# Performance work log

Hardware: AMD Instinct MI355X
Metric: run time of the kernel (lower is better)

The kernel has to match this reference:

```python
import jax, jax.numpy as jnp
import numpy as np

B, NQ, NK = 2, 4096, 4096
DQ = DK = DV = 256
H = 8
DH = DV // H  # 32
LN_EPS = 1e-5


def _layer_norm(x, gamma, beta):
    mu = jnp.mean(x, axis=-1, keepdims=True)
    var = jnp.var(x, axis=-1, keepdims=True)
    return (x - mu) * jax.lax.rsqrt(var + LN_EPS) * gamma + beta


def setup_inputs() -> dict:
    key = jax.random.key(0)
    ks = jax.random.split(key, 12)
    s = 0.02
    return {
        "Q": jax.random.normal(ks[0], (B, NQ, DQ), jnp.float32),
        "K": jax.random.normal(ks[1], (B, NK, DK), jnp.float32),
        "Wq": jax.random.normal(ks[2], (DV, DQ), jnp.float32) * s,
        "bq": jnp.zeros((DV,), jnp.float32),
        "Wk": jax.random.normal(ks[3], (DV, DK), jnp.float32) * s,
        "bk": jnp.zeros((DV,), jnp.float32),
        "Wv": jax.random.normal(ks[4], (DV, DK), jnp.float32) * s,
        "bv": jnp.zeros((DV,), jnp.float32),
        "Wo": jax.random.normal(ks[5], (DV, DV), jnp.float32) * s,
        "bo": jnp.zeros((DV,), jnp.float32),
        "g0": jnp.ones((DV,), jnp.float32),
        "beta0": jnp.zeros((DV,), jnp.float32),
        "g1": jnp.ones((DV,), jnp.float32),
        "beta1": jnp.zeros((DV,), jnp.float32),
    }


def reference(Q, K, Wq, bq, Wk, bk, Wv, bv, Wo, bo, g0, beta0, g1, beta1):
    # dropout is identity in eval mode
    b, nq, _ = Q.shape
    nk = K.shape[1]
    Qp = (Q @ Wq.T + bq).reshape(b, nq, H, DH)
    Kp = (K @ Wk.T + bk).reshape(b, nk, H, DH)
    Vp = (K @ Wv.T + bv).reshape(b, nk, H, DH)
    scale = 1.0 / np.sqrt(DH).astype(np.float32)
    scores = jnp.einsum("bqhd,bkhd->bhqk", Qp, Kp) * scale
    attn = jax.nn.softmax(scores, axis=-1)
    out = jnp.einsum("bhqk,bkhd->bqhd", attn, Vp).reshape(b, nq, DV)
    out = out @ Wo.T + bo
    out = _layer_norm(out, g0, beta0)
    out = _layer_norm(out + jax.nn.relu(out), g1, beta1)
    return out
```

## Files before the change

### kernel.cpp

```cpp
#include <hip/hip_runtime.h>
#include <hip/hip_bf16.h>
#include <math.h>


typedef __attribute__((ext_vector_type(4))) float f32x4;
typedef __attribute__((ext_vector_type(16))) float f32x16;
typedef __attribute__((ext_vector_type(8))) short s16x8;
typedef __attribute__((ext_vector_type(2))) unsigned u32x2;

#define MFMA_BF16(A, B, C) __builtin_amdgcn_mfma_f32_16x16x32_bf16((A), (B), (C), 0, 0, 0)
#define MFMA32(A, B, C) __builtin_amdgcn_mfma_f32_32x32x16_bf16((A), (B), (C), 0, 0, 0)

static __device__ __forceinline__ unsigned short f2bf(float f) {
    union { float f; unsigned u; } v; v.f = f;
    unsigned u = v.u;
    unsigned r = (u + 0x7FFFu + ((u >> 16) & 1u)) >> 16;
    return (unsigned short)r;
}

static __device__ __forceinline__ float bf2f(unsigned short b) {
    union { unsigned u; float f; } v; v.u = ((unsigned)b) << 16;
    return v.f;
}

static __device__ __forceinline__ unsigned cvtpk(float lo, float hi) {
    unsigned r;
    asm("v_cvt_pk_bf16_f32 %0, %1, %2" : "=v"(r) : "v"(lo), "v"(hi));
    return r;
}

static __device__ __forceinline__ s16x8 mk8(unsigned a, unsigned b, unsigned c, unsigned d) {
    union { unsigned u[4]; s16x8 v; } x;
    x.u[0] = a; x.u[1] = b; x.u[2] = c; x.u[3] = d;
    return x.v;
}

__global__ __launch_bounds__(256) void k_cvt_all(
    const float* __restrict__ K,
    const float* __restrict__ Wq, const float* __restrict__ Wk,
    const float* __restrict__ Wv, const float* __restrict__ Wo,
    unsigned short* __restrict__ Kb,
    unsigned short* __restrict__ Wqf, unsigned short* __restrict__ Wkf,
    unsigned short* __restrict__ Wvf, unsigned short* __restrict__ Wof) {
    int bid = blockIdx.x, tid = threadIdx.x;
    if (bid < 2048) {
        int idx = bid * 256 + tid;
        float4 v = ((const float4*)K)[idx];
        ushort4 o;
        o.x = f2bf(v.x); o.y = f2bf(v.y); o.z = f2bf(v.z); o.w = f2bf(v.w);
        ((ushort4*)Kb)[idx] = o;
    } else {
        int w = (bid - 2048) >> 6;
        const float* src = (w == 0) ? Wq : (w == 1) ? Wk : (w == 2) ? Wv : Wo;
        unsigned short* dst = (w == 0) ? Wqf : (w == 1) ? Wkf : (w == 2) ? Wvf : Wof;
        int idx = ((bid - 2048) & 63) * 256 + tid;
        int s = idx * 4;
        int row = s >> 8, col = s & 255;
        float4 v = ((const float4*)src)[idx];
        size_t d = (size_t)(row >> 4) * 4096 + ((size_t)(col >> 5) << 9) +
                   (((col >> 3) & 3) << 7) + ((row & 15) << 3) + (col & 7);
        ushort4 o;
        o.x = f2bf(v.x); o.y = f2bf(v.y); o.z = f2bf(v.z); o.w = f2bf(v.w);
        *(ushort4*)(dst + d) = o;
    }
}

__global__ __launch_bounds__(128) void k_proj(
    const float* __restrict__ Qf, const unsigned short* __restrict__ Kb,
    const unsigned short* __restrict__ Wqf, const unsigned short* __restrict__ Wkf,
    const unsigned short* __restrict__ Wvf,
    const float* __restrict__ bq, const float* __restrict__ bk, const float* __restrict__ bv,
    unsigned short* __restrict__ Qp, unsigned short* __restrict__ Kf,
    unsigned short* __restrict__ Vf, float qscale) {
    __shared__ unsigned short lds[2][16][256];
    const int wv = threadIdx.x >> 6, lid = threadIdx.x & 63;
    const int i = lid & 15, G = lid >> 4;
    const int bid = blockIdx.x;
    if (bid < 512) {
        const int which = bid >> 8;
        const unsigned short* W = which ? Wkf : Wqf;
        const float* bias = which ? bk : bq;
        const float scale = which ? 1.0f : qscale;
        const int m0 = (bid & 255) * 32 + wv * 16;
        f32x4 acc[16];
#pragma unroll
        for (int nf = 0; nf < 16; ++nf) acc[nf] = f32x4{0.f, 0.f, 0.f, 0.f};
        const unsigned short* Xrow = Kb + (size_t)(m0 + i) * 256;
        const float* Qrow = Qf + (size_t)(m0 + i) * 256;
#pragma unroll
        for (int k0 = 0; k0 < 256; k0 += 32) {
            s16x8 a;
            if (which) {
                a = *(const s16x8*)(Xrow + k0 + G * 8);
            } else {
                float4 f0 = *(const float4*)(Qrow + k0 + G * 8);
                float4 f1 = *(const float4*)(Qrow + k0 + G * 8 + 4);
                a = mk8(cvtpk(f0.x, f0.y), cvtpk(f0.z, f0.w),
                        cvtpk(f1.x, f1.y), cvtpk(f1.z, f1.w));
            }
#pragma unroll
            for (int nf = 0; nf < 16; ++nf) {
                s16x8 b = *(const s16x8*)(W + nf * 4096 + ((k0 >> 5) << 9) + lid * 8);
                acc[nf] = MFMA_BF16(a, b, acc[nf]);
            }
        }
#pragma unroll
        for (int nf = 0; nf < 16; ++nf) {
            int col = nf * 16 + i;
            float bvv = bias[col];
#pragma unroll
            for (int r = 0; r < 4; ++r) {
                lds[wv][G * 4 + r][col] = f2bf((acc[nf][r] + bvv) * scale);
            }
        }
#pragma unroll
        for (int it = 0; it < 8; ++it) {
            int run = it * 64 + lid;
            int row = run >> 5, cg = run & 31;
            int col0 = cg * 8;
            s16x8 v = *(const s16x8*)&lds[wv][row][col0];
            int m = m0 + row;
            int bb = m >> 12, j = m & 4095;
            int h = col0 >> 5, dh0 = col0 & 31;
            if (which == 0) {
                *(s16x8*)(Qp + (size_t)(((bb << 3) + h) * 4096 + j) * 32 + dh0) = v;
            } else {
                size_t off = (size_t)((bb << 3) + h) * 131072 +
                             (size_t)(j >> 5) * 1024 + ((dh0 >> 4) & 1) * 512 +
                             ((j & 31) + ((dh0 >> 3) & 1) * 32) * 8;
                *(s16x8*)(Kf + off) = v;
            }
        }
    } else {
        const int tid = bid - 512;
        const int n0 = (tid & 127) * 64;
        const int dv0 = (tid >> 7) * 32 + wv * 16;
        f32x4 acc[4];
#pragma unroll
        for (int nf = 0; nf < 4; ++nf) acc[nf] = f32x4{0.f, 0.f, 0.f, 0.f};
        const unsigned short* Wvp = Wvf + (size_t)((tid >> 7) * 2 + wv) * 4096;
#pragma unroll
        for (int k0 = 0; k0 < 256; k0 += 32) {
            s16x8 a = *(const s16x8*)(Wvp + ((k0 >> 5) << 9) + lid * 8);
#pragma unroll
            for (int nf = 0; nf < 4; ++nf) {
                s16x8 b = *(const s16x8*)(Kb + (size_t)(n0 + nf * 16 + i) * 256 + k0 + G * 8);
                acc[nf] = MFMA_BF16(a, b, acc[nf]);
            }
        }
#pragma unroll
        for (int r = 0; r < 4; ++r) {
            float bvv = bv[dv0 + G * 4 + r];
#pragma unroll
            for (int nf = 0; nf < 4; ++nf) {
                lds[wv][G * 4 + r][nf * 16 + i] = f2bf(acc[nf][r] + bvv);
            }
        }
#pragma unroll
        for (int it = 0; it < 2; ++it) {
            int run = it * 64 + lid;
            int row = run >> 3, jg = run & 7;
            int j0l = jg * 8;
            s16x8 v = *(const s16x8*)&lds[wv][row][j0l];
            int dv = dv0 + row;
            int j = n0 + j0l;
            int bb = j >> 12, jj = j & 4095;
            int h = dv >> 5, dvl = dv & 31;
            int rem = jj & 31;
            size_t off = (size_t)((bb << 3) + h) * 131072 +
                         (size_t)(jj >> 5) * 1024 + (rem >> 4) * 512 +
                         (size_t)(dvl + ((rem >> 3) & 1) * 32) * 8;
            *(s16x8*)(Vf + off) = v;
        }
    }
}

static __device__ __forceinline__ void sm_tile(f32x16 st, s16x8& pa0, s16x8& pa1) {
#pragma unroll
    for (int r = 0; r < 16; ++r) st[r] = __builtin_amdgcn_exp2f(st[r]);
    unsigned w00 = cvtpk(st[0], st[1]),   w01 = cvtpk(st[2], st[3]);
    unsigned w10 = cvtpk(st[4], st[5]),   w11 = cvtpk(st[6], st[7]);
    unsigned w20 = cvtpk(st[8], st[9]),   w21 = cvtpk(st[10], st[11]);
    unsigned w30 = cvtpk(st[12], st[13]), w31 = cvtpk(st[14], st[15]);
    u32x2 sA0 = __builtin_amdgcn_permlane32_swap(w00, w10, false, false);
    u32x2 sB0 = __builtin_amdgcn_permlane32_swap(w01, w11, false, false);
    u32x2 sA1 = __builtin_amdgcn_permlane32_swap(w20, w30, false, false);
    u32x2 sB1 = __builtin_amdgcn_permlane32_swap(w21, w31, false, false);
    pa0 = mk8(sA0[0], sB0[0], sA0[1], sB0[1]);
    pa1 = mk8(sA1[0], sB1[0], sA1[1], sB1[1]);
}

__global__ __launch_bounds__(256, 4) void k_attn(const unsigned short* __restrict__ Qp,
                                                 const unsigned short* __restrict__ Kf,
                                                 const unsigned short* __restrict__ Vf,
                                                 unsigned short* __restrict__ Ob,
                                                 float* __restrict__ Lb) {
    const int wv = threadIdx.x >> 6, l = threadIdx.x & 63;
    const int ql = l & 31, hi = l >> 5;
    int bid = blockIdx.x;
    int wg = ((bid & 7) << 7) | (bid >> 3);
    int bh = wg >> 6;
    int rest = wg & 63;
    int qblk = rest >> 1, sp = rest & 1;
    const unsigned short* Qh = Qp + (size_t)bh * 4096 * 32;
    const int q0 = qblk * 128 + wv * 32;

    s16x8 qb0 = *(const s16x8*)(Qh + (size_t)(q0 + ql) * 32 + hi * 8);
    s16x8 qb1 = *(const s16x8*)(Qh + (size_t)(q0 + ql) * 32 + 16 + hi * 8);

    f32x16 acc, accL, Z;
#pragma unroll
    for (int r = 0; r < 16; ++r) { acc[r] = 0.f; accL[r] = 0.f; Z[r] = 0.f; }
    const s16x8 ONES = mk8(0x3F803F80u, 0x3F803F80u, 0x3F803F80u, 0x3F803F80u);

    const unsigned short* Kl = Kf + (size_t)bh * 131072 + (size_t)sp * 65536 + l * 8;
    const unsigned short* Vl = Vf + (size_t)bh * 131072 + (size_t)sp * 65536 + l * 8;
    s16x8 kA0 = *(const s16x8*)(Kl + 0),    kA1 = *(const s16x8*)(Kl + 512);
    s16x8 kB0 = *(const s16x8*)(Kl + 1024), kB1 = *(const s16x8*)(Kl + 1536);
    s16x8 vA0 = *(const s16x8*)(Vl + 0),    vA1 = *(const s16x8*)(Vl + 512);
    s16x8 vB0 = *(const s16x8*)(Vl + 1024), vB1 = *(const s16x8*)(Vl + 1536);

    f32x16 st = MFMA32(kA0, qb0, Z);
    st = MFMA32(kA1, qb1, st);
    s16x8 paA0, paA1, paB0, paB1;
    sm_tile(st, paA0, paA1);
    f32x16 stn;

    for (int t = 0; t < 64; t += 2) {
        {
            int t2 = (t + 2 < 64) ? t + 2 : 62;
            stn  = MFMA32(kB0, qb0, Z);
            stn  = MFMA32(kB1, qb1, stn);
            acc  = MFMA32(paA0, vA0, acc);
            acc  = MFMA32(paA1, vA1, acc);
            accL = MFMA32(paA0, ONES, accL);
            accL = MFMA32(paA1, ONES, accL);
            kA0 = *(const s16x8*)(Kl + (size_t)t2 * 1024);
            kA1 = *(const s16x8*)(Kl + (size_t)t2 * 1024 + 512);
            sm_tile(stn, paB0, paB1);
            vA0 = *(const s16x8*)(Vl + (size_t)t2 * 1024);
            vA1 = *(const s16x8*)(Vl + (size_t)t2 * 1024 + 512);
        }
        {
            int t2 = (t + 3 < 64) ? t + 3 : 62;
            stn  = MFMA32(kA0, qb0, Z);
            stn  = MFMA32(kA1, qb1, stn);
            acc  = MFMA32(paB0, vB0, acc);
            acc  = MFMA32(paB1, vB1, acc);
            accL = MFMA32(paB0, ONES, accL);
            accL = MFMA32(paB1, ONES, accL);
            kB0 = *(const s16x8*)(Kl + (size_t)t2 * 1024);
            kB1 = *(const s16x8*)(Kl + (size_t)t2 * 1024 + 512);
            sm_tile(stn, paA0, paA1);
            vB0 = *(const s16x8*)(Vl + (size_t)t2 * 1024);
            vB1 = *(const s16x8*)(Vl + (size_t)t2 * 1024 + 512);
        }
    }

    const int bb = bh >> 3, h = bh & 7;
    unsigned short* Obs = Ob + (size_t)sp * 8192 * 256;
#pragma unroll
    for (int r = 0; r < 16; ++r) {
        int qr = (r & 3) + 8 * (r >> 2) + 4 * hi;
        float o = acc[r] / accL[r];
        Obs[(size_t)((bb << 12) + q0 + qr) * 256 + h * 32 + ql] = f2bf(o);
        if (ql == 0) Lb[(size_t)(sp * 16 + bh) * 4096 + q0 + qr] = accL[r];
    }
}

__global__ __launch_bounds__(128) void k_epi(const unsigned short* __restrict__ Ob,
                                             const float* __restrict__ Lb,
                                             const unsigned short* __restrict__ W,
                                             const float* __restrict__ bo,
                                             const float* __restrict__ g0,
                                             const float* __restrict__ be0,
                                             const float* __restrict__ g1,
                                             const float* __restrict__ be1,
                                             float* __restrict__ out) {
    const int wv = threadIdx.x >> 6, lid = threadIdx.x & 63;
    const int i = lid & 15, G = lid >> 4;
    const int m0 = blockIdx.x * 32 + wv * 16;
    const int mrow = m0 + i;
    const int bb = mrow >> 12, qq = mrow & 4095;
    float lw0[8], lw1[8];
#pragma unroll
    for (int h = 0; h < 8; ++h) {
        float l0 = Lb[(size_t)(bb * 8 + h) * 4096 + qq];
        float l1 = Lb[(size_t)(16 + bb * 8 + h) * 4096 + qq];
        float inv = 1.f / (l0 + l1);
        lw0[h] = l0 * inv;
        lw1[h] = l1 * inv;
    }
    f32x4 acc[16];
#pragma unroll
    for (int nf = 0; nf < 16; ++nf) acc[nf] = f32x4{0.f, 0.f, 0.f, 0.f};
    const unsigned short* A0 = Ob + (size_t)mrow * 256;
    const unsigned short* A1 = Ob + (size_t)8192 * 256 + (size_t)mrow * 256;
#pragma unroll
    for (int k0 = 0; k0 < 256; k0 += 32) {
        int h = k0 >> 5;
        float w0 = lw0[h], w1 = lw1[h];
        s16x8 x0 = *(const s16x8*)(A0 + k0 + G * 8);
        s16x8 x1 = *(const s16x8*)(A1 + k0 + G * 8);
        union { unsigned short us[8]; s16x8 v; } au;
#pragma unroll
        for (int e = 0; e < 8; ++e) {
            float c = bf2f((unsigned short)x0[e]) * w0 + bf2f((unsigned short)x1[e]) * w1;
            au.us[e] = f2bf(c);
        }
        s16x8 a = au.v;
#pragma unroll
        for (int nf = 0; nf < 16; ++nf) {
            s16x8 b = *(const s16x8*)(W + nf * 4096 + ((k0 >> 5) << 9) + lid * 8);
            acc[nf] = MFMA_BF16(a, b, acc[nf]);
        }
    }
    f32x4 s1 = f32x4{0.f, 0.f, 0.f, 0.f}, s2 = f32x4{0.f, 0.f, 0.f, 0.f};
#pragma unroll
    for (int nf = 0; nf < 16; ++nf) {
        float bbv = bo[nf * 16 + i];
#pragma unroll
        for (int r = 0; r < 4; ++r) {
            float x = acc[nf][r] + bbv;
            acc[nf][r] = x;
            s1[r] += x;
            s2[r] += x * x;
        }
    }
#pragma unroll
    for (int mk = 1; mk < 16; mk <<= 1) {
#pragma unroll
        for (int r = 0; r < 4; ++r) {
            s1[r] += __shfl_xor(s1[r], mk);
            s2[r] += __shfl_xor(s2[r], mk);
        }
    }
    f32x4 mu, rs;
#pragma unroll
    for (int r = 0; r < 4; ++r) {
        mu[r] = s1[r] * (1.f / 256.f);
        float var = s2[r] * (1.f / 256.f) - mu[r] * mu[r];
        rs[r] = rsqrtf(var + 1e-5f);
    }
    f32x4 t1 = f32x4{0.f, 0.f, 0.f, 0.f}, t2 = f32x4{0.f, 0.f, 0.f, 0.f};
#pragma unroll
    for (int nf = 0; nf < 16; ++nf) {
        float gv = g0[nf * 16 + i], bv = be0[nf * 16 + i];
#pragma unroll
        for (int r = 0; r < 4; ++r) {
            float y = (acc[nf][r] - mu[r]) * rs[r] * gv + bv;
            float z = y + fmaxf(y, 0.f);
            acc[nf][r] = z;
            t1[r] += z;
            t2[r] += z * z;
        }
    }
#pragma unroll
    for (int mk = 1; mk < 16; mk <<= 1) {
#pragma unroll
        for (int r = 0; r < 4; ++r) {
            t1[r] += __shfl_xor(t1[r], mk);
            t2[r] += __shfl_xor(t2[r], mk);
        }
    }
    f32x4 mu2, rs2;
#pragma unroll
    for (int r = 0; r < 4; ++r) {
        mu2[r] = t1[r] * (1.f / 256.f);
        float var = t2[r] * (1.f / 256.f) - mu2[r] * mu2[r];
        rs2[r] = rsqrtf(var + 1e-5f);
    }
#pragma unroll
    for (int nf = 0; nf < 16; ++nf) {
        int col = nf * 16 + i;
        float gv = g1[col], bv = be1[col];
#pragma unroll
        for (int r = 0; r < 4; ++r) {
            out[(size_t)(m0 + G * 4 + r) * 256 + col] = (acc[nf][r] - mu2[r]) * rs2[r] * gv + bv;
        }
    }
}

extern "C" void kernel_launch(void* const* d_in, const int* in_sizes, int n_in,
                              void* d_out, int out_size, void* d_ws, size_t ws_size,
                              hipStream_t stream) {
    const float* Q   = (const float*)d_in[0];
    const float* K   = (const float*)d_in[1];
    const float* Wq  = (const float*)d_in[2];
    const float* bq  = (const float*)d_in[3];
    const float* Wk  = (const float*)d_in[4];
    const float* bk  = (const float*)d_in[5];
    const float* Wv  = (const float*)d_in[6];
    const float* bv  = (const float*)d_in[7];
    const float* Wo  = (const float*)d_in[8];
    const float* bo  = (const float*)d_in[9];
    const float* g0  = (const float*)d_in[10];
    const float* be0 = (const float*)d_in[11];
    const float* g1  = (const float*)d_in[12];
    const float* be1 = (const float*)d_in[13];
    float* out = (float*)d_out;

    char* ws = (char*)d_ws;
    unsigned short* Wqf = (unsigned short*)(ws + (size_t)0);
    unsigned short* Wkf = (unsigned short*)(ws + ((size_t)128 << 10));
    unsigned short* Wvf = (unsigned short*)(ws + ((size_t)256 << 10));
    unsigned short* Wof = (unsigned short*)(ws + ((size_t)384 << 10));
    size_t off = (size_t)512 << 10;
    const size_t big = (size_t)8192 * 256 * 2;
    unsigned short* Kb = (unsigned short*)(ws + off); off += big;
    unsigned short* Qp = (unsigned short*)(ws + off); off += big;
    unsigned short* Kf = (unsigned short*)(ws + off); off += big;
    unsigned short* Vf = (unsigned short*)(ws + off); off += big;
    unsigned short* Oa = (unsigned short*)(ws + off); off += big;
    unsigned short* Ob = (unsigned short*)(ws + off); off += 2 * big;
    float* Lb = (float*)(ws + off); off += (size_t)2 * 16 * 4096 * 4;
    (void)Oa;

    k_cvt_all<<<2304, 256, 0, stream>>>(K, Wq, Wk, Wv, Wo,
                                        Kb, Wqf, Wkf, Wvf, Wof);

    const float qscale = 1.4426950408889634f / sqrtf(32.0f);
    k_proj<<<1536, 128, 0, stream>>>(Q, Kb, Wqf, Wkf, Wvf, bq, bk, bv,
                                     Qp, Kf, Vf, qscale);

    k_attn<<<1024, 256, 0, stream>>>(Qp, Kf, Vf, Ob, Lb);

    k_epi<<<256, 128, 0, stream>>>(Ob, Lb, Wof, bo, g0, be0, g1, be1, out);
}
```

Before: 100.8 us.

## Split epilogue output columns across two waves with shared-memory LayerNorm reduction

The epilogue kernel now gives each block 16 rows instead of 32, and its two waves split the 256 output columns in half. LayerNorm statistics are combined across the waves through a small shared-memory buffer and block barriers. This doubles the grid to 512 blocks so the epilogue fills more compute units and halves each wave's accumulator registers. In exchange it adds three barriers and loads the combined A tile redundantly in both waves.

Result: no change. 99.08 us (-1.7%).

```diff
diff --git a/kernel.cpp b/kernel.cpp
--- a/kernel.cpp
+++ b/kernel.cpp
@@ -277,9 +277,10 @@
                                              const float* __restrict__ g1,
                                              const float* __restrict__ be1,
                                              float* __restrict__ out) {
+    __shared__ float red[2][2][16];
     const int wv = threadIdx.x >> 6, lid = threadIdx.x & 63;
     const int i = lid & 15, G = lid >> 4;
-    const int m0 = blockIdx.x * 32 + wv * 16;
+    const int m0 = blockIdx.x * 16;
     const int mrow = m0 + i;
     const int bb = mrow >> 12, qq = mrow & 4095;
     float lw0[8], lw1[8];
@@ -291,9 +292,9 @@
         lw0[h] = l0 * inv;
         lw1[h] = l1 * inv;
     }
-    f32x4 acc[16];
-#pragma unroll
-    for (int nf = 0; nf < 16; ++nf) acc[nf] = f32x4{0.f, 0.f, 0.f, 0.f};
+    f32x4 acc[8];
+#pragma unroll
+    for (int nf8 = 0; nf8 < 8; ++nf8) acc[nf8] = f32x4{0.f, 0.f, 0.f, 0.f};
     const unsigned short* A0 = Ob + (size_t)mrow * 256;
     const unsigned short* A1 = Ob + (size_t)8192 * 256 + (size_t)mrow * 256;
 #pragma unroll
@@ -310,19 +311,20 @@
         }
         s16x8 a = au.v;
 #pragma unroll
-        for (int nf = 0; nf < 16; ++nf) {
+        for (int nf8 = 0; nf8 < 8; ++nf8) {
+            int nf = wv * 8 + nf8;
             s16x8 b = *(const s16x8*)(W + nf * 4096 + ((k0 >> 5) << 9) + lid * 8);
-            acc[nf] = MFMA_BF16(a, b, acc[nf]);
+            acc[nf8] = MFMA_BF16(a, b, acc[nf8]);
         }
     }
     f32x4 s1 = f32x4{0.f, 0.f, 0.f, 0.f}, s2 = f32x4{0.f, 0.f, 0.f, 0.f};
 #pragma unroll
-    for (int nf = 0; nf < 16; ++nf) {
-        float bbv = bo[nf * 16 + i];
-#pragma unroll
-        for (int r = 0; r < 4; ++r) {
-            float x = acc[nf][r] + bbv;
-            acc[nf][r] = x;
+    for (int nf8 = 0; nf8 < 8; ++nf8) {
+        float bbv = bo[(wv * 8 + nf8) * 16 + i];
+#pragma unroll
+        for (int r = 0; r < 4; ++r) {
+            float x = acc[nf8][r] + bbv;
+            acc[nf8][r] = x;
             s1[r] += x;
             s2[r] += x * x;
         }
@@ -335,22 +337,34 @@
             s2[r] += __shfl_xor(s2[r], mk);
         }
     }
+    if (i == 0) {
+#pragma unroll
+        for (int r = 0; r < 4; ++r) {
+            red[wv][0][G * 4 + r] = s1[r];
+            red[wv][1][G * 4 + r] = s2[r];
+        }
+    }
+    __syncthreads();
     f32x4 mu, rs;
 #pragma unroll
     for (int r = 0; r < 4; ++r) {
-        mu[r] = s1[r] * (1.f / 256.f);
-        float var = s2[r] * (1.f / 256.f) - mu[r] * mu[r];
+        float S1 = red[0][0][G * 4 + r] + red[1][0][G * 4 + r];
+        float S2 = red[0][1][G * 4 + r] + red[1][1][G * 4 + r];
+        mu[r] = S1 * (1.f / 256.f);
+        float var = S2 * (1.f / 256.f) - mu[r] * mu[r];
         rs[r] = rsqrtf(var + 1e-5f);
     }
+    __syncthreads();
     f32x4 t1 = f32x4{0.f, 0.f, 0.f, 0.f}, t2 = f32x4{0.f, 0.f, 0.f, 0.f};
 #pragma unroll
-    for (int nf = 0; nf < 16; ++nf) {
-        float gv = g0[nf * 16 + i], bv = be0[nf * 16 + i];
-#pragma unroll
-        for (int r = 0; r < 4; ++r) {
-            float y = (acc[nf][r] - mu[r]) * rs[r] * gv + bv;
+    for (int nf8 = 0; nf8 < 8; ++nf8) {
+        int col = (wv * 8 + nf8) * 16 + i;
+        float gv = g0[col], bv = be0[col];
+#pragma unroll
+        for (int r = 0; r < 4; ++r) {
+            float y = (acc[nf8][r] - mu[r]) * rs[r] * gv + bv;
             float z = y + fmaxf(y, 0.f);
-            acc[nf][r] = z;
+            acc[nf8][r] = z;
             t1[r] += z;
             t2[r] += z * z;
         }
@@ -363,20 +377,30 @@
             t2[r] += __shfl_xor(t2[r], mk);
         }
     }
+    if (i == 0) {
+#pragma unroll
+        for (int r = 0; r < 4; ++r) {
+            red[wv][0][G * 4 + r] = t1[r];
+            red[wv][1][G * 4 + r] = t2[r];
+        }
+    }
+    __syncthreads();
     f32x4 mu2, rs2;
 #pragma unroll
     for (int r = 0; r < 4; ++r) {
-        mu2[r] = t1[r] * (1.f / 256.f);
-        float var = t2[r] * (1.f / 256.f) - mu2[r] * mu2[r];
+        float T1 = red[0][0][G * 4 + r] + red[1][0][G * 4 + r];
+        float T2 = red[0][1][G * 4 + r] + red[1][1][G * 4 + r];
+        mu2[r] = T1 * (1.f / 256.f);
+        float var = T2 * (1.f / 256.f) - mu2[r] * mu2[r];
         rs2[r] = rsqrtf(var + 1e-5f);
     }
 #pragma unroll
-    for (int nf = 0; nf < 16; ++nf) {
-        int col = nf * 16 + i;
+    for (int nf8 = 0; nf8 < 8; ++nf8) {
+        int col = (wv * 8 + nf8) * 16 + i;
         float gv = g1[col], bv = be1[col];
 #pragma unroll
         for (int r = 0; r < 4; ++r) {
-            out[(size_t)(m0 + G * 4 + r) * 256 + col] = (acc[nf][r] - mu2[r]) * rs2[r] * gv + bv;
+            out[(size_t)(m0 + G * 4 + r) * 256 + col] = (acc[nf8][r] - mu2[r]) * rs2[r] * gv + bv;
         }
     }
 }
@@ -425,5 +449,5 @@
 
     k_attn<<<1024, 256, 0, stream>>>(Qp, Kf, Vf, Ob, Lb);
 
-    k_epi<<<256, 128, 0, stream>>>(Ob, Lb, Wof, bo, g0, be0, g1, be1, out);
-}
+    k_epi<<<512, 128, 0, stream>>>(Ob, Lb, Wof, bo, g0, be0, g1, be1, out);
+}
```
